# Performance work log

Measured on AMD Instinct MI355X. Metric: run time of the kernel, lower is better.

## Reference

```python
import jax, jax.numpy as jnp
import numpy as np

R, N1, N2, D = 4, 4096, 4096, 8


def setup_inputs() -> dict:
    key = jax.random.key(0)
    k1, k2, k3 = jax.random.split(key, 3)
    x1 = jax.random.normal(k1, (R, N1, D), dtype=jnp.float32)
    x2 = jax.random.normal(k2, (R, N2, D), dtype=jnp.float32)
    # learned parameters (init: ones), matching nn.Parameter(torch.ones(...))
    lengthscales = jnp.ones((D, 1), dtype=jnp.float32)
    output_scale = jnp.ones((1,), dtype=jnp.float32)
    return {"x1": x1, "x2": x2, "lengthscales": lengthscales, "output_scale": output_scale}


def reference(x1, x2, lengthscales, output_scale):
    # RBF.K: output_scale^2 * exp(-0.5 * sum_d ((x1 - x2) / lengthscales)^2)
    # Computed via the Gram identity ||a-b||^2 = ||a||^2 + ||b||^2 - 2 a.b
    inv_ls = 1.0 / lengthscales.reshape(-1)          # [D]
    a = x1 * inv_ls                                  # [R, N1, D]
    b = x2 * inv_ls                                  # [R, N2, D]
    aa = jnp.sum(a * a, axis=-1)                     # [R, N1]
    bb = jnp.sum(b * b, axis=-1)                     # [R, N2]
    ab = jnp.einsum('rnd,rmd->rnm', a, b)            # [R, N1, N2]
    sqdist = jnp.maximum(aa[:, :, None] + bb[:, None, :] - 2.0 * ab, 0.0)
    return (output_scale[0] ** 2) * jnp.exp(-0.5 * sqdist)
```

## Files before the change

### kernel.cpp

```cpp
#include <hip/hip_runtime.h>


constexpr int D  = 8;
constexpr int BI = 32;
constexpr int BJ = 512;

#if __has_builtin(__builtin_amdgcn_exp2f)
#define FAST_EXP2(x) __builtin_amdgcn_exp2f(x)
#else
#define FAST_EXP2(x) __expf((x) * 0.69314718f)
#endif

__global__ __launch_bounds__(256, 4) void rbf_kernel(
    const float* __restrict__ x1, const float* __restrict__ x2,
    const float* __restrict__ ls, const float* __restrict__ osc,
    float* __restrict__ out, int N1, int N2)
{
    __shared__ float sb[D][BJ];
    __shared__ float sbb[BJ];
    __shared__ float sa[BI][D];
    __shared__ float sasq[BI];

    const int r   = blockIdx.z;
    const int i0  = blockIdx.y * BI;
    const int j0  = blockIdx.x * BJ;
    const int tid = threadIdx.x;

    float4 l0 = *reinterpret_cast<const float4*>(ls);
    float4 l1 = *reinterpret_cast<const float4*>(ls + 4);
    float4 inv0, inv1;
    inv0.x = 1.0f / l0.x; inv0.y = 1.0f / l0.y; inv0.z = 1.0f / l0.z; inv0.w = 1.0f / l0.w;
    inv1.x = 1.0f / l1.x; inv1.y = 1.0f / l1.y; inv1.z = 1.0f / l1.z; inv1.w = 1.0f / l1.w;

#pragma unroll
    for (int k = 0; k < 2; ++k) {
        const int p = k * 256 + tid;
        const float* src = x2 + ((size_t)r * N2 + j0 + p) * D;
        float4 v0 = *reinterpret_cast<const float4*>(src);
        float4 v1 = *reinterpret_cast<const float4*>(src + 4);
        v0.x *= inv0.x; v0.y *= inv0.y; v0.z *= inv0.z; v0.w *= inv0.w;
        v1.x *= inv1.x; v1.y *= inv1.y; v1.z *= inv1.z; v1.w *= inv1.w;
        sb[0][p] = v0.x; sb[1][p] = v0.y; sb[2][p] = v0.z; sb[3][p] = v0.w;
        sb[4][p] = v1.x; sb[5][p] = v1.y; sb[6][p] = v1.z; sb[7][p] = v1.w;
        sbb[p] = v0.x*v0.x + v0.y*v0.y + v0.z*v0.z + v0.w*v0.w
               + v1.x*v1.x + v1.y*v1.y + v1.z*v1.z + v1.w*v1.w;
    }
    if (tid < BI) {
        const float* src = x1 + ((size_t)r * N1 + i0 + tid) * D;
        float4 v0 = *reinterpret_cast<const float4*>(src);
        float4 v1 = *reinterpret_cast<const float4*>(src + 4);
        v0.x *= inv0.x; v0.y *= inv0.y; v0.z *= inv0.z; v0.w *= inv0.w;
        v1.x *= inv1.x; v1.y *= inv1.y; v1.z *= inv1.z; v1.w *= inv1.w;
        *reinterpret_cast<float4*>(&sa[tid][0]) = v0;
        *reinterpret_cast<float4*>(&sa[tid][4]) = v1;
        sasq[tid] = v0.x*v0.x + v0.y*v0.y + v0.z*v0.z + v0.w*v0.w
                  + v1.x*v1.x + v1.y*v1.y + v1.z*v1.z + v1.w*v1.w;
    }
    const float os2   = osc[0] * osc[0];
    const float lg2os = __log2f(os2);
    __syncthreads();

    const int lane = tid & 63;
    const int wv   = tid >> 6;

    float4 bd0[D], bd1[D];
#pragma unroll
    for (int d = 0; d < D; ++d) {
        bd0[d] = *reinterpret_cast<const float4*>(&sb[d][lane * 4]);
        bd1[d] = *reinterpret_cast<const float4*>(&sb[d][256 + lane * 4]);
    }
    const float4 bbA = *reinterpret_cast<const float4*>(&sbb[lane * 4]);
    const float4 bbB = *reinterpret_cast<const float4*>(&sbb[256 + lane * 4]);

    constexpr float L2E  = 1.44269504f;
    constexpr float NH2E = -0.72134752f;

    float4 cb0, cb1;
    cb0.x = fmaf(bbA.x, NH2E, lg2os); cb0.y = fmaf(bbA.y, NH2E, lg2os);
    cb0.z = fmaf(bbA.z, NH2E, lg2os); cb0.w = fmaf(bbA.w, NH2E, lg2os);
    cb1.x = fmaf(bbB.x, NH2E, lg2os); cb1.y = fmaf(bbB.y, NH2E, lg2os);
    cb1.z = fmaf(bbB.z, NH2E, lg2os); cb1.w = fmaf(bbB.w, NH2E, lg2os);

    float* obase = out + ((size_t)r * N1 + i0) * (size_t)N2 + j0 + lane * 4;

#pragma unroll
    for (int ii = 0; ii < 8; ++ii) {
        const int row = wv * 8 + ii;
        const float4 a0  = *reinterpret_cast<const float4*>(&sa[row][0]);
        const float4 a1  = *reinterpret_cast<const float4*>(&sa[row][4]);
        const float  ca  = sasq[row] * NH2E;

        float p0 = 0.f, p1 = 0.f, p2 = 0.f, p3 = 0.f;
        float q0 = 0.f, q1 = 0.f, q2 = 0.f, q3 = 0.f;
        const float a[D] = {a0.x, a0.y, a0.z, a0.w, a1.x, a1.y, a1.z, a1.w};
#pragma unroll
        for (int d = 0; d < D; ++d) {
            const float av = a[d];
            p0 = fmaf(av, bd0[d].x, p0);
            p1 = fmaf(av, bd0[d].y, p1);
            p2 = fmaf(av, bd0[d].z, p2);
            p3 = fmaf(av, bd0[d].w, p3);
            q0 = fmaf(av, bd1[d].x, q0);
            q1 = fmaf(av, bd1[d].y, q1);
            q2 = fmaf(av, bd1[d].z, q2);
            q3 = fmaf(av, bd1[d].w, q3);
        }
        float4 oA, oB;
        oA.x = FAST_EXP2(fmaf(p0, L2E, ca + cb0.x));
        oA.y = FAST_EXP2(fmaf(p1, L2E, ca + cb0.y));
        oA.z = FAST_EXP2(fmaf(p2, L2E, ca + cb0.z));
        oA.w = FAST_EXP2(fmaf(p3, L2E, ca + cb0.w));
        oB.x = FAST_EXP2(fmaf(q0, L2E, ca + cb1.x));
        oB.y = FAST_EXP2(fmaf(q1, L2E, ca + cb1.y));
        oB.z = FAST_EXP2(fmaf(q2, L2E, ca + cb1.z));
        oB.w = FAST_EXP2(fmaf(q3, L2E, ca + cb1.w));
        float* op = obase + (size_t)row * N2;
        *reinterpret_cast<float4*>(op)       = oA;
        *reinterpret_cast<float4*>(op + 256) = oB;
    }
}

extern "C" void kernel_launch(void* const* d_in, const int* in_sizes, int n_in,
                              void* d_out, int out_size, void* d_ws, size_t ws_size,
                              hipStream_t stream) {
    (void)in_sizes; (void)n_in; (void)d_ws; (void)ws_size; (void)out_size;
    const float* x1  = (const float*)d_in[0];
    const float* x2  = (const float*)d_in[1];
    const float* ls  = (const float*)d_in[2];
    const float* osc = (const float*)d_in[3];
    float* out = (float*)d_out;

    const int R = 4, N1 = 4096, N2 = 4096;
    dim3 grid(N2 / BJ, N1 / BI, R);
    rbf_kernel<<<grid, dim3(256), 0, stream>>>(x1, x2, ls, osc, out, N1, N2);
}
```

Measured before the change: 47.54 us.

## Process multiple row tiles per block and read x1 rows directly from global

Each block now covers four consecutive 32-row tiles, so the x2 tile staged in shared memory and its norms are reused across 128 output rows instead of 32. The x1 rows are loaded straight from global memory per row and scaled in registers, removing the shared staging of x1 and its norms. This cuts per-block setup and the grid size fourfold, at the cost of fewer blocks for load balancing and per-row global loads in the inner loop.

```diff
diff --git a/kernel.cpp b/kernel.cpp
--- a/kernel.cpp
+++ b/kernel.cpp
@@ -3,6 +3,7 @@
 
 constexpr int D  = 8;
 constexpr int BI = 32;
+constexpr int IT = 4;
 constexpr int BJ = 512;
 
 #if __has_builtin(__builtin_amdgcn_exp2f)
@@ -18,11 +19,9 @@
 {
     __shared__ float sb[D][BJ];
     __shared__ float sbb[BJ];
-    __shared__ float sa[BI][D];
-    __shared__ float sasq[BI];
 
     const int r   = blockIdx.z;
-    const int i0  = blockIdx.y * BI;
+    const int i0  = blockIdx.y * (BI * IT);
     const int j0  = blockIdx.x * BJ;
     const int tid = threadIdx.x;
 
@@ -44,17 +43,6 @@
         sb[4][p] = v1.x; sb[5][p] = v1.y; sb[6][p] = v1.z; sb[7][p] = v1.w;
         sbb[p] = v0.x*v0.x + v0.y*v0.y + v0.z*v0.z + v0.w*v0.w
                + v1.x*v1.x + v1.y*v1.y + v1.z*v1.z + v1.w*v1.w;
-    }
-    if (tid < BI) {
-        const float* src = x1 + ((size_t)r * N1 + i0 + tid) * D;
-        float4 v0 = *reinterpret_cast<const float4*>(src);
-        float4 v1 = *reinterpret_cast<const float4*>(src + 4);
-        v0.x *= inv0.x; v0.y *= inv0.y; v0.z *= inv0.z; v0.w *= inv0.w;
-        v1.x *= inv1.x; v1.y *= inv1.y; v1.z *= inv1.z; v1.w *= inv1.w;
-        *reinterpret_cast<float4*>(&sa[tid][0]) = v0;
-        *reinterpret_cast<float4*>(&sa[tid][4]) = v1;
-        sasq[tid] = v0.x*v0.x + v0.y*v0.y + v0.z*v0.z + v0.w*v0.w
-                  + v1.x*v1.x + v1.y*v1.y + v1.z*v1.z + v1.w*v1.w;
     }
     const float os2   = osc[0] * osc[0];
     const float lg2os = __log2f(os2);
@@ -82,41 +70,55 @@
     cb1.z = fmaf(bbB.z, NH2E, lg2os); cb1.w = fmaf(bbB.w, NH2E, lg2os);
 
     float* obase = out + ((size_t)r * N1 + i0) * (size_t)N2 + j0 + lane * 4;
+    const float* x1base = x1 + ((size_t)r * N1 + i0) * D;
 
+#pragma unroll 4
+    for (int t = 0; t < IT; ++t) {
 #pragma unroll
-    for (int ii = 0; ii < 8; ++ii) {
-        const int row = wv * 8 + ii;
-        const float4 a0  = *reinterpret_cast<const float4*>(&sa[row][0]);
-        const float4 a1  = *reinterpret_cast<const float4*>(&sa[row][4]);
-        const float  ca  = sasq[row] * NH2E;
+        for (int ii = 0; ii < 8; ++ii) {
+            const int row = t * BI + wv * 8 + ii;
+            const float* xp = x1base + (size_t)row * D;
+            float a[D];
+            float asq = 0.f;
+            {
+                const float4 u0 = *reinterpret_cast<const float4*>(xp);
+                const float4 u1 = *reinterpret_cast<const float4*>(xp + 4);
+                a[0] = u0.x * inv0.x; a[1] = u0.y * inv0.y;
+                a[2] = u0.z * inv0.z; a[3] = u0.w * inv0.w;
+                a[4] = u1.x * inv1.x; a[5] = u1.y * inv1.y;
+                a[6] = u1.z * inv1.z; a[7] = u1.w * inv1.w;
+#pragma unroll
+                for (int d = 0; d < D; ++d) asq = fmaf(a[d], a[d], asq);
+            }
+            const float ca = asq * NH2E;
 
-        float p0 = 0.f, p1 = 0.f, p2 = 0.f, p3 = 0.f;
-        float q0 = 0.f, q1 = 0.f, q2 = 0.f, q3 = 0.f;
-        const float a[D] = {a0.x, a0.y, a0.z, a0.w, a1.x, a1.y, a1.z, a1.w};
+            float p0 = 0.f, p1 = 0.f, p2 = 0.f, p3 = 0.f;
+            float q0 = 0.f, q1 = 0.f, q2 = 0.f, q3 = 0.f;
 #pragma unroll
-        for (int d = 0; d < D; ++d) {
-            const float av = a[d];
-            p0 = fmaf(av, bd0[d].x, p0);
-            p1 = fmaf(av, bd0[d].y, p1);
-            p2 = fmaf(av, bd0[d].z, p2);
-            p3 = fmaf(av, bd0[d].w, p3);
-            q0 = fmaf(av, bd1[d].x, q0);
-            q1 = fmaf(av, bd1[d].y, q1);
-            q2 = fmaf(av, bd1[d].z, q2);
-            q3 = fmaf(av, bd1[d].w, q3);
+            for (int d = 0; d < D; ++d) {
+                const float av = a[d];
+                p0 = fmaf(av, bd0[d].x, p0);
+                p1 = fmaf(av, bd0[d].y, p1);
+                p2 = fmaf(av, bd0[d].z, p2);
+                p3 = fmaf(av, bd0[d].w, p3);
+                q0 = fmaf(av, bd1[d].x, q0);
+                q1 = fmaf(av, bd1[d].y, q1);
+                q2 = fmaf(av, bd1[d].z, q2);
+                q3 = fmaf(av, bd1[d].w, q3);
+            }
+            float4 oA, oB;
+            oA.x = FAST_EXP2(fmaf(p0, L2E, ca + cb0.x));
+            oA.y = FAST_EXP2(fmaf(p1, L2E, ca + cb0.y));
+            oA.z = FAST_EXP2(fmaf(p2, L2E, ca + cb0.z));
+            oA.w = FAST_EXP2(fmaf(p3, L2E, ca + cb0.w));
+            oB.x = FAST_EXP2(fmaf(q0, L2E, ca + cb1.x));
+            oB.y = FAST_EXP2(fmaf(q1, L2E, ca + cb1.y));
+            oB.z = FAST_EXP2(fmaf(q2, L2E, ca + cb1.z));
+            oB.w = FAST_EXP2(fmaf(q3, L2E, ca + cb1.w));
+            float* op = obase + (size_t)row * N2;
+            *reinterpret_cast<float4*>(op)       = oA;
+            *reinterpret_cast<float4*>(op + 256) = oB;
         }
-        float4 oA, oB;
-        oA.x = FAST_EXP2(fmaf(p0, L2E, ca + cb0.x));
-        oA.y = FAST_EXP2(fmaf(p1, L2E, ca + cb0.y));
-        oA.z = FAST_EXP2(fmaf(p2, L2E, ca + cb0.z));
-        oA.w = FAST_EXP2(fmaf(p3, L2E, ca + cb0.w));
-        oB.x = FAST_EXP2(fmaf(q0, L2E, ca + cb1.x));
-        oB.y = FAST_EXP2(fmaf(q1, L2E, ca + cb1.y));
-        oB.z = FAST_EXP2(fmaf(q2, L2E, ca + cb1.z));
-        oB.w = FAST_EXP2(fmaf(q3, L2E, ca + cb1.w));
-        float* op = obase + (size_t)row * N2;
-        *reinterpret_cast<float4*>(op)       = oA;
-        *reinterpret_cast<float4*>(op + 256) = oB;
     }
 }
 
@@ -131,6 +133,6 @@
     float* out = (float*)d_out;
 
     const int R = 4, N1 = 4096, N2 = 4096;
-    dim3 grid(N2 / BJ, N1 / BI, R);
+    dim3 grid(N2 / BJ, N1 / (BI * IT), R);
     rbf_kernel<<<grid, dim3(256), 0, stream>>>(x1, x2, ls, osc, out, N1, N2);
 }
```

Measured after the change: 47.25 us (median of 2 runs). Within noise of the previous version (-0.6%).
